# Optimization experiments

Measured on AMD Instinct MI355X. Metric: run time of the kernel, lower is better.

Reference implementation:

```python
import jax, jax.numpy as jnp
import numpy as np

N, C_IN, C_OUT, L, V, P, K, STRIDE = 8, 256, 256, 512, 25, 3, 9, 1
BN_EPS = 1e-5


def setup_inputs() -> dict:
    key = jax.random.key(0)
    k1, k2, k3, k4, k5 = jax.random.split(key, 5)
    x = jax.random.normal(k1, (N, C_IN, L, V), dtype=jnp.float32)
    # 1x1 Conv2d weight, no bias: (out_channels*num_partitions, in_channels)
    conv_w = jax.random.normal(k2, (C_OUT * P, C_IN), dtype=jnp.float32) * (1.0 / np.sqrt(C_IN))
    # adjacency (P, V, V)
    A = jax.random.normal(k3, (P, V, V), dtype=jnp.float32) * 0.2
    bn_gamma = jnp.ones((C_OUT,), dtype=jnp.float32)
    bn_beta = jnp.zeros((C_OUT,), dtype=jnp.float32)
    bn_mean = jax.random.normal(k4, (C_OUT,), dtype=jnp.float32) * 0.1
    bn_var = jax.random.uniform(k5, (C_OUT,), dtype=jnp.float32) + 0.5
    return {"x": x, "conv_w": conv_w, "A": A, "bn_gamma": bn_gamma,
            "bn_beta": bn_beta, "bn_mean": bn_mean, "bn_var": bn_var}


def reference(x, conv_w, A, bn_gamma, bn_beta, bn_mean, bn_var):
    # residual branch: identity (in_channels == out_channels, stride == 1)
    res = x
    # 1x1 conv: (N, C_in, L, V) -> (N, C_out*P, L, V)
    y = jnp.einsum('nclv,oc->nolv', x, conv_w)
    # split channels into P partitions, stack, permute -> (N, L, P, C_out, V)
    y = y.reshape(N, P, C_OUT, L, V).transpose(0, 3, 1, 2, 4)
    # graph aggregation: x @ A per partition
    y = jnp.einsum('nlpcv,pvw->nlpcw', y, A)
    # sum over partitions -> (N, L, C_out, V)
    s = y.sum(axis=2)
    # FIFO with zero init + strided taps == causal strided window sum:
    # out[t] = sum_{k=0}^{K-1} s[t - k*STRIDE], zero-padded for t-k*STRIDE < 0
    pad = (K - 1) * STRIDE
    s_pad = jnp.pad(s, ((0, 0), (pad, 0), (0, 0), (0, 0)))
    out = s_pad[:, 0:L]
    for k in range(1, K):
        out = out + s_pad[:, k * STRIDE:k * STRIDE + L]
    # stack along dim 2 in torch -> (N, C_out, L, V)
    out = out.transpose(0, 2, 1, 3)
    # BatchNorm2d (eval, running stats) + ReLU
    scale = bn_gamma * jax.lax.rsqrt(bn_var + BN_EPS)
    shift = bn_beta - bn_mean * scale
    out = out * scale[None, :, None, None] + shift[None, :, None, None]
    out = jax.nn.relu(out)
    # residual add, then ReLU (Dropout p=0.0 is identity)
    out = jax.nn.relu(out + res)
    return out
```

## Files before the change

### kernel.cpp

```cpp
#include <hip/hip_runtime.h>
#include <hip/hip_bf16.h>

#define NB 8
#define CC 256
#define OO 768
#define LL 512
#define VV 25
#define PP 3
#define KM 768
#define NKC 24
#define LT 4

typedef __attribute__((ext_vector_type(8))) short short8v;
typedef __attribute__((ext_vector_type(4))) float float4v;
typedef __attribute__((ext_vector_type(4))) int int4v;

__device__ inline unsigned pk2(float a, float b){
    __hip_bfloat16 ha = __float2bfloat16(a), hb = __float2bfloat16(b);
    unsigned short ua = *(unsigned short*)&ha, ub = *(unsigned short*)&hb;
    return (unsigned)ua | ((unsigned)ub << 16);
}

__global__ __launch_bounds__(256) void wperm_kernel(const float* __restrict__ W,
                                                    __hip_bfloat16* __restrict__ Wp) {
    int idx = blockIdx.x * 256 + threadIdx.x;
    if (idx >= OO * CC) return;
    int j    = idx & 7;
    int lane = (idx >> 3) & 63;
    int mt   = (idx >> 9) & 3;
    int wm   = (idx >> 11) & 3;
    int kc   = idx >> 13;
    int c = wm * 64 + mt * 16 + (lane & 15);
    int k = kc * 32 + ((lane >> 4) << 3) + j;
    int cib = k / 192;
    int r = k - cib * 192;
    int p = r >> 6;
    int ci = cib * 64 + (r & 63);
    Wp[idx] = __float2bfloat16(W[(p * 256 + c) * 256 + ci]);
}

__global__ __launch_bounds__(512, 4) void fused_main_kernel(
    const float* __restrict__ x,
    const __hip_bfloat16* __restrict__ Wp,
    const float* __restrict__ A,
    const float* __restrict__ gamma, const float* __restrict__ beta,
    const float* __restrict__ mean, const float* __restrict__ var,
    float* __restrict__ out)
{
    __shared__ __hip_bfloat16 Zb[2][128 * 32];
    __shared__ __hip_bfloat16 xsh[256 * 32];
    __shared__ __hip_bfloat16 a2t[3 * 32 * 32];
    __shared__ float scsh[512];

    const int tid  = threadIdx.x;
    const int lane = tid & 63, wid = tid >> 6;
    const int lcol = lane & 15, grp = lane >> 4;
    const int bid0 = blockIdx.x;
    const int swz = (bid0 & 7) * 128 + (bid0 >> 3);
    const int n  = swz >> 7;
    const int l0 = (swz & 127) * LT;
    const int wm = wid >> 1, wn = wid & 1;
    const int l_z = wid >> 1, mt_z = wid & 1;

    {
        int4v z = {0, 0, 0, 0};
        ((int4v*)xsh)[tid] = z;
        ((int4v*)xsh)[tid + 512] = z;
        if (tid < 384) ((int4v*)a2t)[tid] = z;
        int c = tid & 255;
        float sc = gamma[c] * rsqrtf(var[c] + 1e-5f);
        if (tid < 256) scsh[tid] = sc;
        else           scsh[tid] = beta[c] - mean[c] * sc;
    }
    __syncthreads();
    for (int idx = tid; idx < PP * VV * VV; idx += 512) {
        int p = idx / 625, r = idx - p * 625, v = r / 25, w = r - v * 25;
        int R = p * 32 + w;
        int e = (((v >> 3) ^ ((R >> 1) & 3)) << 3) | (v & 7);
        a2t[R * 32 + e] = __float2bfloat16(A[idx]);
    }

    auto stage_xs = [&](int cib) {
        for (int cc = tid; cc < 1600; cc += 512) {
            int ci6 = cc / 25, v = cc - ci6 * 25;
            const float* xp = x + ((size_t)(n * CC + cib * 64 + ci6) * LL) * VV + v;
            float rbuf[12];
            #pragma unroll
            for (int j = 0; j < 12; ++j) {
                int lj = l0 - 8 + j;
                rbuf[j] = (lj >= 0) ? xp[(size_t)lj * VV] : 0.f;
            }
            float wsv = 0.f;
            #pragma unroll
            for (int j = 0; j < 9; ++j) wsv += rbuf[j];
            #pragma unroll
            for (int i = 0; i < 4; ++i) {
                int R = ci6 * 4 + i;
                int e = (((v >> 3) ^ ((R >> 2) & 3)) << 3) | (v & 7);
                xsh[R * 32 + e] = __float2bfloat16(wsv);
                if (i < 3) wsv += rbuf[9 + i] - rbuf[i];
            }
        }
    };
    auto zgen = [&](int kc, int zbuf) {
        int p = (kc % 6) >> 1, h = kc & 1;
        int ci6 = h * 32 + mt_z * 16 + lcol;
        int R = ci6 * 4 + l_z;
        short8v az = *(const short8v*)&xsh[R * 32 + ((grp ^ ((R >> 2) & 3)) << 3)];
        #pragma unroll
        for (int wt = 0; wt < 2; ++wt) {
            int R2 = p * 32 + wt * 16 + lcol;
            short8v bz = *(const short8v*)&a2t[R2 * 32 + ((grp ^ ((R2 >> 1) & 3)) << 3)];
            float4v zc = {0.f, 0.f, 0.f, 0.f};
            zc = __builtin_amdgcn_mfma_f32_16x16x32_bf16(az, bz, zc, 0, 0, 0);
            int R3 = l_z * 32 + wt * 16 + lcol;
            int eb = (mt_z * 2 + (grp >> 1)) ^ ((R3 >> 1) & 3);
            unsigned* dst = (unsigned*)&Zb[zbuf][R3 * 32 + (eb << 3) + ((grp & 1) << 2)];
            dst[0] = pk2(zc[0], zc[1]);
            dst[1] = pk2(zc[2], zc[3]);
        }
    };

    float4v acc[4][4];
    #pragma unroll
    for (int i = 0; i < 4; ++i)
        #pragma unroll
        for (int j = 0; j < 4; ++j) acc[i][j] = (float4v){0.f, 0.f, 0.f, 0.f};

    const __hip_bfloat16* afbase = Wp + ((size_t)(wm * 4) * 64 + lane) * 8;

    #pragma unroll 1
    for (int cib = 0; cib < 4; ++cib) {
        stage_xs(cib);
        asm volatile("s_waitcnt lgkmcnt(0)" ::: "memory");
        __builtin_amdgcn_sched_barrier(0);
        __builtin_amdgcn_s_barrier();
        __builtin_amdgcn_sched_barrier(0);

        zgen(cib * 6, (cib * 6) & 1);
        asm volatile("s_waitcnt lgkmcnt(0)" ::: "memory");
        __builtin_amdgcn_sched_barrier(0);
        __builtin_amdgcn_s_barrier();
        __builtin_amdgcn_sched_barrier(0);

        #pragma unroll 1
        for (int j = 0; j < 6; ++j) {
            const int kc = cib * 6 + j;

            short8v af[4];
            {
                const __hip_bfloat16* ap = afbase + kc * 8192;
                #pragma unroll
                for (int mt = 0; mt < 4; ++mt)
                    af[mt] = *(const short8v*)(ap + mt * 512);
            }

            if (j < 5) zgen(kc + 1, (kc + 1) & 1);

            const __hip_bfloat16* zcur = &Zb[kc & 1][0];
            short8v bf[4];
            #pragma unroll
            for (int nt = 0; nt < 4; ++nt) {
                int R3 = wn * 64 + nt * 16 + lcol;
                bf[nt] = *(const short8v*)&zcur[R3 * 32 + ((grp ^ ((R3 >> 1) & 3)) << 3)];
            }

            __builtin_amdgcn_s_setprio(1);
            #pragma unroll
            for (int mt = 0; mt < 4; ++mt)
                #pragma unroll
                for (int nt = 0; nt < 4; ++nt)
                    acc[mt][nt] = __builtin_amdgcn_mfma_f32_16x16x32_bf16(af[mt], bf[nt], acc[mt][nt], 0, 0, 0);
            __builtin_amdgcn_s_setprio(0);

            asm volatile("s_waitcnt lgkmcnt(0)" ::: "memory");
            __builtin_amdgcn_sched_barrier(0);
            __builtin_amdgcn_s_barrier();
            __builtin_amdgcn_sched_barrier(0);
        }
    }

    #pragma unroll
    for (int mt = 0; mt < 4; ++mt) {
        #pragma unroll
        for (int nt = 0; nt < 4; ++nt) {
            int w = (wn * 64 + nt * 16) & 31;
            int l = l0 + ((wn * 64 + nt * 16) >> 5);
            int wl = w + lcol;
            if (wl < VV) {
                #pragma unroll
                for (int r = 0; r < 4; ++r) {
                    int c = wm * 64 + mt * 16 + grp * 4 + r;
                    float val = fmaf(acc[mt][nt][r], scsh[c], scsh[256 + c]);
                    val = fmaxf(val, 0.f);
                    size_t ad = ((size_t)(n * CC + c) * LL + l) * VV + wl;
                    val = fmaxf(val + x[ad], 0.f);
                    out[ad] = val;
                }
            }
        }
    }
}

__global__ __launch_bounds__(256) void wsum_kernel(const float* __restrict__ x,
                                                   float* __restrict__ xs) {
    const int CHUNKS = 8;
    int t = blockIdx.x * 256 + threadIdx.x;
    if (t >= NB * CC * VV * CHUNKS) return;
    int v = t % VV;
    int r = t / VV;
    int chunk = r % CHUNKS;
    int nc = r / CHUNKS;
    int l0 = chunk * (LL / CHUNKS);
    const float* xp = x  + (size_t)nc * (LL * VV) + v;
    float*       op = xs + (size_t)nc * (LL * VV) + v;
    float ring[8];
    float run = 0.f;
    #pragma unroll
    for (int k = 0; k < 8; ++k) {
        int j = l0 - 8 + k;
        float val = (j >= 0) ? xp[j * VV] : 0.f;
        ring[k] = val; run += val;
    }
    for (int base = l0; base < l0 + LL / CHUNKS; base += 8) {
        #pragma unroll
        for (int k = 0; k < 8; ++k) {
            int l = base + k;
            float val = xp[l * VV];
            float o = run + val;
            op[l * VV] = o;
            run = o - ring[k];
            ring[k] = val;
        }
    }
}

__global__ __launch_bounds__(256) void fused_fallback_kernel(
    const float* xs, const float* __restrict__ x, const float* __restrict__ W,
    const float* __restrict__ A,
    const float* __restrict__ gamma, const float* __restrict__ beta,
    const float* __restrict__ mean, const float* __restrict__ var,
    float* out)
{
    __shared__ float xshf[CC][28];
    const int bid = blockIdx.x;
    const int n = bid >> 9;
    const int l = bid & 511;
    const int tid = threadIdx.x;
    const size_t nbase = (size_t)n * CC * LL * VV;
    for (int k = tid; k < CC * VV; k += 256) {
        int ci = k / VV, v = k - ci * VV;
        xshf[ci][v] = xs[nbase + (size_t)ci * (LL * VV) + (size_t)l * VV + v];
    }
    __syncthreads();
    const int c = tid;
    float Y[PP * VV];
    #pragma unroll
    for (int i = 0; i < PP * VV; ++i) Y[i] = 0.f;
    const float* Wpr = W + c * 256;
    #pragma unroll 1
    for (int ci = 0; ci < CC; ++ci) {
        float xv[VV];
        #pragma unroll
        for (int v = 0; v < VV; ++v) xv[v] = xshf[ci][v];
        float w0 = Wpr[ci], w1 = Wpr[65536 + ci], w2 = Wpr[131072 + ci];
        #pragma unroll
        for (int v = 0; v < VV; ++v) Y[v]          = fmaf(w0, xv[v], Y[v]);
        #pragma unroll
        for (int v = 0; v < VV; ++v) Y[VV + v]     = fmaf(w1, xv[v], Y[VV + v]);
        #pragma unroll
        for (int v = 0; v < VV; ++v) Y[2 * VV + v] = fmaf(w2, xv[v], Y[2 * VV + v]);
    }
    float o[VV];
    #pragma unroll
    for (int w = 0; w < VV; ++w) o[w] = 0.f;
    #pragma unroll
    for (int p = 0; p < PP; ++p)
        #pragma unroll
        for (int v = 0; v < VV; ++v) {
            float y = Y[p * VV + v];
            const float* Ap = A + (p * VV + v) * VV;
            #pragma unroll
            for (int w = 0; w < VV; ++w) o[w] = fmaf(y, Ap[w], o[w]);
        }
    float sc = gamma[c] * rsqrtf(var[c] + 1e-5f);
    float sh = beta[c] - mean[c] * sc;
    const float* resp = x   + nbase + (size_t)c * (LL * VV) + (size_t)l * VV;
    float*       outp = out + nbase + (size_t)c * (LL * VV) + (size_t)l * VV;
    #pragma unroll
    for (int w = 0; w < VV; ++w) {
        float t2 = fmaf(o[w], sc, sh);
        t2 = fmaxf(t2, 0.f);
        t2 = fmaxf(t2 + resp[w], 0.f);
        outp[w] = t2;
    }
}

extern "C" void kernel_launch(void* const* d_in, const int* in_sizes, int n_in,
                              void* d_out, int out_size, void* d_ws, size_t ws_size,
                              hipStream_t stream) {
    const float* x  = (const float*)d_in[0];
    const float* W  = (const float*)d_in[1];
    const float* A  = (const float*)d_in[2];
    const float* gm = (const float*)d_in[3];
    const float* bt = (const float*)d_in[4];
    const float* mn = (const float*)d_in[5];
    const float* vr = (const float*)d_in[6];
    float* out = (float*)d_out;

    if (ws_size >= (size_t)(OO * CC * sizeof(__hip_bfloat16))) {
        __hip_bfloat16* Wp = (__hip_bfloat16*)d_ws;
        wperm_kernel<<<dim3((OO * CC + 255) / 256), dim3(256), 0, stream>>>(W, Wp);
        fused_main_kernel<<<dim3(NB * (LL / LT)), dim3(512), 0, stream>>>(
            x, Wp, A, gm, bt, mn, vr, out);
    } else {
        const int threadsA = NB * CC * VV * 8;
        wsum_kernel<<<dim3((threadsA + 255) / 256), dim3(256), 0, stream>>>(x, out);
        fused_fallback_kernel<<<dim3(NB * LL), dim3(256), 0, stream>>>(
            out, x, W, A, gm, bt, mn, vr, out);
    }
}
```

Before: 107.3 us.

## Halve L tile per block, use 4 waves, and double-buffer weight fragment loads

Each block now covers two time steps instead of four and runs 256 threads, with each of the four waves owning 64 output channels across the whole 64-column tile. This doubles the grid to 2048 blocks and roughly halves LDS use per block. Weight fragments for the next k-step are prefetched into a second register set while the current MFMAs run, and the setprio hints and trailing sched barriers are dropped. In exchange, each weight tile is reused across half as many columns, so weight traffic per output roughly doubles and more blocks re-read the x window halo.

```diff
diff --git a/kernel.cpp b/kernel.cpp
--- a/kernel.cpp
+++ b/kernel.cpp
@@ -9,7 +9,7 @@
 #define PP 3
 #define KM 768
 #define NKC 24
-#define LT 4
+#define LT 2
 
 typedef __attribute__((ext_vector_type(8))) short short8v;
 typedef __attribute__((ext_vector_type(4))) float float4v;
@@ -39,7 +39,7 @@
     Wp[idx] = __float2bfloat16(W[(p * 256 + c) * 256 + ci]);
 }
 
-__global__ __launch_bounds__(512, 4) void fused_main_kernel(
+__global__ __launch_bounds__(256, 4) void fused_main_kernel(
     const float* __restrict__ x,
     const __hip_bfloat16* __restrict__ Wp,
     const float* __restrict__ A,
@@ -47,8 +47,8 @@
     const float* __restrict__ mean, const float* __restrict__ var,
     float* __restrict__ out)
 {
-    __shared__ __hip_bfloat16 Zb[2][128 * 32];
-    __shared__ __hip_bfloat16 xsh[256 * 32];
+    __shared__ __hip_bfloat16 Zb[2][64 * 32];
+    __shared__ __hip_bfloat16 xsh[128 * 32];
     __shared__ __hip_bfloat16 a2t[3 * 32 * 32];
     __shared__ float scsh[512];
 
@@ -56,24 +56,24 @@
     const int lane = tid & 63, wid = tid >> 6;
     const int lcol = lane & 15, grp = lane >> 4;
     const int bid0 = blockIdx.x;
-    const int swz = (bid0 & 7) * 128 + (bid0 >> 3);
-    const int n  = swz >> 7;
-    const int l0 = (swz & 127) * LT;
-    const int wm = wid >> 1, wn = wid & 1;
-    const int l_z = wid >> 1, mt_z = wid & 1;
+    const int swz = (bid0 & 7) * 256 + (bid0 >> 3);
+    const int n  = swz >> 8;
+    const int l0 = (swz & 255) * LT;
+    const int wm = wid;
+    const int mt_z = wid & 1, l_z = wid >> 1;
 
     {
         int4v z = {0, 0, 0, 0};
         ((int4v*)xsh)[tid] = z;
-        ((int4v*)xsh)[tid + 512] = z;
-        if (tid < 384) ((int4v*)a2t)[tid] = z;
-        int c = tid & 255;
-        float sc = gamma[c] * rsqrtf(var[c] + 1e-5f);
-        if (tid < 256) scsh[tid] = sc;
-        else           scsh[tid] = beta[c] - mean[c] * sc;
+        ((int4v*)xsh)[tid + 256] = z;
+        ((int4v*)a2t)[tid] = z;
+        if (tid < 128) ((int4v*)a2t)[tid + 256] = z;
+        float sc = gamma[tid] * rsqrtf(var[tid] + 1e-5f);
+        scsh[tid] = sc;
+        scsh[256 + tid] = beta[tid] - mean[tid] * sc;
     }
     __syncthreads();
-    for (int idx = tid; idx < PP * VV * VV; idx += 512) {
+    for (int idx = tid; idx < PP * VV * VV; idx += 256) {
         int p = idx / 625, r = idx - p * 625, v = r / 25, w = r - v * 25;
         int R = p * 32 + w;
         int e = (((v >> 3) ^ ((R >> 1) & 3)) << 3) | (v & 7);
@@ -81,12 +81,12 @@
     }
 
     auto stage_xs = [&](int cib) {
-        for (int cc = tid; cc < 1600; cc += 512) {
+        for (int cc = tid; cc < 1600; cc += 256) {
             int ci6 = cc / 25, v = cc - ci6 * 25;
             const float* xp = x + ((size_t)(n * CC + cib * 64 + ci6) * LL) * VV + v;
-            float rbuf[12];
+            float rbuf[10];
             #pragma unroll
-            for (int j = 0; j < 12; ++j) {
+            for (int j = 0; j < 10; ++j) {
                 int lj = l0 - 8 + j;
                 rbuf[j] = (lj >= 0) ? xp[(size_t)lj * VV] : 0.f;
             }
@@ -94,19 +94,19 @@
             #pragma unroll
             for (int j = 0; j < 9; ++j) wsv += rbuf[j];
             #pragma unroll
-            for (int i = 0; i < 4; ++i) {
-                int R = ci6 * 4 + i;
-                int e = (((v >> 3) ^ ((R >> 2) & 3)) << 3) | (v & 7);
+            for (int i = 0; i < LT; ++i) {
+                int R = ci6 * LT + i;
+                int e = (((v >> 3) ^ ((R >> 1) & 3)) << 3) | (v & 7);
                 xsh[R * 32 + e] = __float2bfloat16(wsv);
-                if (i < 3) wsv += rbuf[9 + i] - rbuf[i];
+                if (i < LT - 1) wsv += rbuf[9 + i] - rbuf[i];
             }
         }
     };
     auto zgen = [&](int kc, int zbuf) {
         int p = (kc % 6) >> 1, h = kc & 1;
         int ci6 = h * 32 + mt_z * 16 + lcol;
-        int R = ci6 * 4 + l_z;
-        short8v az = *(const short8v*)&xsh[R * 32 + ((grp ^ ((R >> 2) & 3)) << 3)];
+        int R = ci6 * LT + l_z;
+        short8v az = *(const short8v*)&xsh[R * 32 + ((grp ^ ((R >> 1) & 3)) << 3)];
         #pragma unroll
         for (int wt = 0; wt < 2; ++wt) {
             int R2 = p * 32 + wt * 16 + lcol;
@@ -129,63 +129,64 @@
 
     const __hip_bfloat16* afbase = Wp + ((size_t)(wm * 4) * 64 + lane) * 8;
 
+#define KSTEP(kc, j, afc, afn) do {                                           \
+    if ((kc) + 1 < NKC) {                                                     \
+        const __hip_bfloat16* ap_ = afbase + (size_t)((kc) + 1) * 8192;       \
+        _Pragma("unroll")                                                     \
+        for (int mt_ = 0; mt_ < 4; ++mt_)                                     \
+            afn[mt_] = *(const short8v*)(ap_ + mt_ * 512);                    \
+    }                                                                         \
+    if ((j) < 5) zgen((kc) + 1, ((kc) + 1) & 1);                              \
+    {                                                                         \
+        const __hip_bfloat16* zcur_ = &Zb[(kc) & 1][0];                       \
+        short8v bf_[4];                                                       \
+        _Pragma("unroll")                                                     \
+        for (int nt_ = 0; nt_ < 4; ++nt_) {                                   \
+            int R3_ = nt_ * 16 + lcol;                                        \
+            bf_[nt_] = *(const short8v*)&zcur_[R3_ * 32 + ((grp ^ ((R3_ >> 1) & 3)) << 3)]; \
+        }                                                                     \
+        _Pragma("unroll")                                                     \
+        for (int mt_ = 0; mt_ < 4; ++mt_)                                     \
+            _Pragma("unroll")                                                 \
+            for (int nt_ = 0; nt_ < 4; ++nt_)                                 \
+                acc[mt_][nt_] = __builtin_amdgcn_mfma_f32_16x16x32_bf16(afc[mt_], bf_[nt_], acc[mt_][nt_], 0, 0, 0); \
+    }                                                                         \
+    asm volatile("s_waitcnt lgkmcnt(0)" ::: "memory");                        \
+    __builtin_amdgcn_sched_barrier(0);                                        \
+    __builtin_amdgcn_s_barrier();                                             \
+} while (0)
+
+    short8v afA[4], afB[4];
+    #pragma unroll
+    for (int mt = 0; mt < 4; ++mt) afA[mt] = *(const short8v*)(afbase + mt * 512);
+
     #pragma unroll 1
     for (int cib = 0; cib < 4; ++cib) {
         stage_xs(cib);
         asm volatile("s_waitcnt lgkmcnt(0)" ::: "memory");
         __builtin_amdgcn_sched_barrier(0);
         __builtin_amdgcn_s_barrier();
-        __builtin_amdgcn_sched_barrier(0);
 
         zgen(cib * 6, (cib * 6) & 1);
         asm volatile("s_waitcnt lgkmcnt(0)" ::: "memory");
         __builtin_amdgcn_sched_barrier(0);
         __builtin_amdgcn_s_barrier();
-        __builtin_amdgcn_sched_barrier(0);
 
         #pragma unroll 1
-        for (int j = 0; j < 6; ++j) {
-            const int kc = cib * 6 + j;
-
-            short8v af[4];
-            {
-                const __hip_bfloat16* ap = afbase + kc * 8192;
-                #pragma unroll
-                for (int mt = 0; mt < 4; ++mt)
-                    af[mt] = *(const short8v*)(ap + mt * 512);
-            }
-
-            if (j < 5) zgen(kc + 1, (kc + 1) & 1);
-
-            const __hip_bfloat16* zcur = &Zb[kc & 1][0];
-            short8v bf[4];
-            #pragma unroll
-            for (int nt = 0; nt < 4; ++nt) {
-                int R3 = wn * 64 + nt * 16 + lcol;
-                bf[nt] = *(const short8v*)&zcur[R3 * 32 + ((grp ^ ((R3 >> 1) & 3)) << 3)];
-            }
-
-            __builtin_amdgcn_s_setprio(1);
-            #pragma unroll
-            for (int mt = 0; mt < 4; ++mt)
-                #pragma unroll
-                for (int nt = 0; nt < 4; ++nt)
-                    acc[mt][nt] = __builtin_amdgcn_mfma_f32_16x16x32_bf16(af[mt], bf[nt], acc[mt][nt], 0, 0, 0);
-            __builtin_amdgcn_s_setprio(0);
-
-            asm volatile("s_waitcnt lgkmcnt(0)" ::: "memory");
-            __builtin_amdgcn_sched_barrier(0);
-            __builtin_amdgcn_s_barrier();
-            __builtin_amdgcn_sched_barrier(0);
-        }
-    }
+        for (int jj = 0; jj < 3; ++jj) {
+            KSTEP(cib * 6 + jj * 2,     jj * 2,     afA, afB);
+            KSTEP(cib * 6 + jj * 2 + 1, jj * 2 + 1, afB, afA);
+        }
+    }
+#undef KSTEP
 
     #pragma unroll
     for (int mt = 0; mt < 4; ++mt) {
         #pragma unroll
         for (int nt = 0; nt < 4; ++nt) {
-            int w = (wn * 64 + nt * 16) & 31;
-            int l = l0 + ((wn * 64 + nt * 16) >> 5);
+            int lw = nt * 16;
+            int w = lw & 31;
+            int l = l0 + (lw >> 5);
             int wl = w + lcol;
             if (wl < VV) {
                 #pragma unroll
@@ -311,7 +312,7 @@
     if (ws_size >= (size_t)(OO * CC * sizeof(__hip_bfloat16))) {
         __hip_bfloat16* Wp = (__hip_bfloat16*)d_ws;
         wperm_kernel<<<dim3((OO * CC + 255) / 256), dim3(256), 0, stream>>>(W, Wp);
-        fused_main_kernel<<<dim3(NB * (LL / LT)), dim3(512), 0, stream>>>(
+        fused_main_kernel<<<dim3(NB * (LL / LT)), dim3(256), 0, stream>>>(
             x, Wp, A, gm, bt, mn, vr, out);
     } else {
         const int threadsA = NB * CC * VV * 8;
```

New measurement: 115.1 us. 1.07x slower.

## Software-pipeline x staging and weight fragment loads across K-steps

Applied to the files above, without the earlier changes.

Prefetches the next channel block's x window sums from global memory into registers during the MFMA steps of the current block. The packed results are written to shared memory only after the block finishes, so global latency hides behind compute instead of sitting in a separate staging phase. Weight fragments are double-buffered so the next K-chunk loads while the current one feeds the MFMAs. Register pressure rises, so launch bounds drop from 4 to 3 waves per SIMD, which lowers occupancy.

```diff
diff --git a/kernel.cpp b/kernel.cpp
--- a/kernel.cpp
+++ b/kernel.cpp
@@ -39,7 +39,7 @@
     Wp[idx] = __float2bfloat16(W[(p * 256 + c) * 256 + ci]);
 }
 
-__global__ __launch_bounds__(512, 4) void fused_main_kernel(
+__global__ __launch_bounds__(512, 3) void fused_main_kernel(
     const float* __restrict__ x,
     const __hip_bfloat16* __restrict__ Wp,
     const float* __restrict__ A,
@@ -94,16 +94,15 @@
             #pragma unroll
             for (int j = 0; j < 9; ++j) wsv += rbuf[j];
             #pragma unroll
-            for (int i = 0; i < 4; ++i) {
+            for (int i = 0; i < LT; ++i) {
                 int R = ci6 * 4 + i;
                 int e = (((v >> 3) ^ ((R >> 2) & 3)) << 3) | (v & 7);
                 xsh[R * 32 + e] = __float2bfloat16(wsv);
-                if (i < 3) wsv += rbuf[9 + i] - rbuf[i];
+                if (i < LT - 1) wsv += rbuf[9 + i] - rbuf[i];
             }
         }
     };
-    auto zgen = [&](int kc, int zbuf) {
-        int p = (kc % 6) >> 1, h = kc & 1;
+    auto zgen = [&](int p, int h, int zbuf) {
         int ci6 = h * 32 + mt_z * 16 + lcol;
         int R = ci6 * 4 + l_z;
         short8v az = *(const short8v*)&xsh[R * 32 + ((grp ^ ((R >> 2) & 3)) << 3)];
@@ -128,64 +127,124 @@
         for (int j = 0; j < 4; ++j) acc[i][j] = (float4v){0.f, 0.f, 0.f, 0.f};
 
     const __hip_bfloat16* afbase = Wp + ((size_t)(wm * 4) * 64 + lane) * 8;
+    unsigned q[8];
+    short8v afA[4], afB[4];
+
+    stage_xs(0);
+    asm volatile("s_waitcnt lgkmcnt(0)" ::: "memory");
+    __builtin_amdgcn_sched_barrier(0);
+    __builtin_amdgcn_s_barrier();
+
+    zgen(0, 0, 0);
+    #pragma unroll
+    for (int mt = 0; mt < 4; ++mt) afA[mt] = *(const short8v*)(afbase + mt * 512);
+    asm volatile("s_waitcnt lgkmcnt(0)" ::: "memory");
+    __builtin_amdgcn_sched_barrier(0);
+    __builtin_amdgcn_s_barrier();
+
+#define KSTEP(J, IT, AFC, AFN) do {                                           \
+    const int kc_ = base + (J);                                               \
+    if (kc_ + 1 < NKC) {                                                      \
+        const __hip_bfloat16* ap_ = afbase + (size_t)(kc_ + 1) * 8192;        \
+        _Pragma("unroll")                                                     \
+        for (int mt_ = 0; mt_ < 4; ++mt_)                                     \
+            AFN[mt_] = *(const short8v*)(ap_ + mt_ * 512);                    \
+    }                                                                         \
+    float rb_[12]; int ci6_ = 0, v_ = 0; bool act_ = false;                   \
+    if ((IT) >= 0 && cib < 3) {                                               \
+        int cc_ = tid + (IT) * 512; act_ = cc_ < 1600;                        \
+        if (act_) {                                                           \
+            ci6_ = cc_ / 25; v_ = cc_ - ci6_ * 25;                            \
+            const float* xp_ = x + ((size_t)(n * CC + (cib + 1) * 64 + ci6_) * LL) * VV + v_; \
+            _Pragma("unroll")                                                 \
+            for (int jx_ = 0; jx_ < 12; ++jx_) {                              \
+                int lj_ = l0 - 8 + jx_;                                       \
+                rb_[jx_] = (lj_ >= 0) ? xp_[(size_t)lj_ * VV] : 0.f;          \
+            }                                                                 \
+        }                                                                     \
+    }                                                                         \
+    if ((J) < 5) zgen((((J) + 1) >> 1) & 3, ((J) + 1) & 1, ((J) + 1) & 1);    \
+    {                                                                         \
+        const __hip_bfloat16* zcur_ = &Zb[(J) & 1][0];                        \
+        short8v bf_[4];                                                       \
+        _Pragma("unroll")                                                     \
+        for (int nt_ = 0; nt_ < 4; ++nt_) {                                   \
+            int R3_ = wn * 64 + nt_ * 16 + lcol;                              \
+            bf_[nt_] = *(const short8v*)&zcur_[R3_ * 32 + ((grp ^ ((R3_ >> 1) & 3)) << 3)]; \
+        }                                                                     \
+        __builtin_amdgcn_s_setprio(1);                                        \
+        _Pragma("unroll")                                                     \
+        for (int mt_ = 0; mt_ < 4; ++mt_)                                     \
+            _Pragma("unroll")                                                 \
+            for (int nt_ = 0; nt_ < 4; ++nt_)                                 \
+                acc[mt_][nt_] = __builtin_amdgcn_mfma_f32_16x16x32_bf16(AFC[mt_], bf_[nt_], acc[mt_][nt_], 0, 0, 0); \
+        __builtin_amdgcn_s_setprio(0);                                        \
+    }                                                                         \
+    if ((IT) >= 0 && act_) {                                                  \
+        float w0_ = 0.f;                                                      \
+        _Pragma("unroll")                                                     \
+        for (int jx_ = 0; jx_ < 9; ++jx_) w0_ += rb_[jx_];                    \
+        float w1_ = w0_ + rb_[9]  - rb_[0];                                   \
+        float w2_ = w1_ + rb_[10] - rb_[1];                                   \
+        float w3_ = w2_ + rb_[11] - rb_[2];                                   \
+        q[(IT) * 2]     = pk2(w0_, w1_);                                      \
+        q[(IT) * 2 + 1] = pk2(w2_, w3_);                                      \
+    }                                                                         \
+    asm volatile("s_waitcnt lgkmcnt(0)" ::: "memory");                        \
+    __builtin_amdgcn_sched_barrier(0);                                        \
+    __builtin_amdgcn_s_barrier();                                             \
+} while (0)
 
     #pragma unroll 1
     for (int cib = 0; cib < 4; ++cib) {
-        stage_xs(cib);
-        asm volatile("s_waitcnt lgkmcnt(0)" ::: "memory");
-        __builtin_amdgcn_sched_barrier(0);
-        __builtin_amdgcn_s_barrier();
-        __builtin_amdgcn_sched_barrier(0);
-
-        zgen(cib * 6, (cib * 6) & 1);
-        asm volatile("s_waitcnt lgkmcnt(0)" ::: "memory");
-        __builtin_amdgcn_sched_barrier(0);
-        __builtin_amdgcn_s_barrier();
-        __builtin_amdgcn_sched_barrier(0);
-
-        #pragma unroll 1
-        for (int j = 0; j < 6; ++j) {
-            const int kc = cib * 6 + j;
-
-            short8v af[4];
-            {
-                const __hip_bfloat16* ap = afbase + kc * 8192;
-                #pragma unroll
-                for (int mt = 0; mt < 4; ++mt)
-                    af[mt] = *(const short8v*)(ap + mt * 512);
+        const int base = cib * 6;
+        KSTEP(0, -1, afA, afB);
+        KSTEP(1,  0, afB, afA);
+        KSTEP(2,  1, afA, afB);
+        KSTEP(3,  2, afB, afA);
+        KSTEP(4,  3, afA, afB);
+        KSTEP(5, -1, afB, afA);
+
+        if (cib < 3) {
+            #pragma unroll
+            for (int it = 0; it < 4; ++it) {
+                int cc = tid + it * 512;
+                if (cc < 1600) {
+                    int ci6 = cc / 25, v = cc - ci6 * 25;
+                    unsigned lo = q[it * 2], hi = q[it * 2 + 1];
+                    unsigned short hh0 = (unsigned short)(lo & 0xffff);
+                    unsigned short hh1 = (unsigned short)(lo >> 16);
+                    unsigned short hh2 = (unsigned short)(hi & 0xffff);
+                    unsigned short hh3 = (unsigned short)(hi >> 16);
+                    int e0 = (((v >> 3) ^ (((ci6 * 4 + 0) >> 2) & 3)) << 3) | (v & 7);
+                    *(unsigned short*)&xsh[(ci6 * 4 + 0) * 32 + e0] = hh0;
+                    int e1 = (((v >> 3) ^ (((ci6 * 4 + 1) >> 2) & 3)) << 3) | (v & 7);
+                    *(unsigned short*)&xsh[(ci6 * 4 + 1) * 32 + e1] = hh1;
+                    int e2 = (((v >> 3) ^ (((ci6 * 4 + 2) >> 2) & 3)) << 3) | (v & 7);
+                    *(unsigned short*)&xsh[(ci6 * 4 + 2) * 32 + e2] = hh2;
+                    int e3 = (((v >> 3) ^ (((ci6 * 4 + 3) >> 2) & 3)) << 3) | (v & 7);
+                    *(unsigned short*)&xsh[(ci6 * 4 + 3) * 32 + e3] = hh3;
+                }
             }
-
-            if (j < 5) zgen(kc + 1, (kc + 1) & 1);
-
-            const __hip_bfloat16* zcur = &Zb[kc & 1][0];
-            short8v bf[4];
-            #pragma unroll
-            for (int nt = 0; nt < 4; ++nt) {
-                int R3 = wn * 64 + nt * 16 + lcol;
-                bf[nt] = *(const short8v*)&zcur[R3 * 32 + ((grp ^ ((R3 >> 1) & 3)) << 3)];
-            }
-
-            __builtin_amdgcn_s_setprio(1);
-            #pragma unroll
-            for (int mt = 0; mt < 4; ++mt)
-                #pragma unroll
-                for (int nt = 0; nt < 4; ++nt)
-                    acc[mt][nt] = __builtin_amdgcn_mfma_f32_16x16x32_bf16(af[mt], bf[nt], acc[mt][nt], 0, 0, 0);
-            __builtin_amdgcn_s_setprio(0);
-
             asm volatile("s_waitcnt lgkmcnt(0)" ::: "memory");
             __builtin_amdgcn_sched_barrier(0);
             __builtin_amdgcn_s_barrier();
+
+            zgen(0, 0, 0);
+            asm volatile("s_waitcnt lgkmcnt(0)" ::: "memory");
             __builtin_amdgcn_sched_barrier(0);
-        }
-    }
+            __builtin_amdgcn_s_barrier();
+        }
+    }
+#undef KSTEP
 
     #pragma unroll
     for (int mt = 0; mt < 4; ++mt) {
         #pragma unroll
         for (int nt = 0; nt < 4; ++nt) {
-            int w = (wn * 64 + nt * 16) & 31;
-            int l = l0 + ((wn * 64 + nt * 16) >> 5);
+            int lw = (wn * 64 + nt * 16);
+            int w = lw & 31;
+            int l = l0 + (lw >> 5);
             int wl = w + lcol;
             if (wl < VV) {
                 #pragma unroll
```

Result: slower. 316.0 us (+194.4%).

## Precompute all six Z tiles per channel block to drop per-step barriers

Applied to the files above, without the earlier changes.

The graph-aggregation tiles for all three partitions and both channel halves are now produced at once into six LDS buffers per input-channel block. This replaces the double-buffered per-step generation, so the six inner GEMM steps run fully unrolled with no barrier between them. The intent is to cut barrier and sync overhead and give the compiler freedom to schedule the MFMA chain. In exchange the kernel uses more LDS, which can lower occupancy under the 512-thread, 4-block launch bound, and Z generation no longer overlaps with the GEMM. The setprio hints are also removed.

```diff
diff --git a/kernel.cpp b/kernel.cpp
--- a/kernel.cpp
+++ b/kernel.cpp
@@ -47,7 +47,7 @@
     const float* __restrict__ mean, const float* __restrict__ var,
     float* __restrict__ out)
 {
-    __shared__ __hip_bfloat16 Zb[2][128 * 32];
+    __shared__ __hip_bfloat16 Zb[6][128 * 32];
     __shared__ __hip_bfloat16 xsh[256 * 32];
     __shared__ __hip_bfloat16 a2t[3 * 32 * 32];
     __shared__ float scsh[512];
@@ -94,30 +94,40 @@
             #pragma unroll
             for (int j = 0; j < 9; ++j) wsv += rbuf[j];
             #pragma unroll
-            for (int i = 0; i < 4; ++i) {
+            for (int i = 0; i < LT; ++i) {
                 int R = ci6 * 4 + i;
                 int e = (((v >> 3) ^ ((R >> 2) & 3)) << 3) | (v & 7);
                 xsh[R * 32 + e] = __float2bfloat16(wsv);
-                if (i < 3) wsv += rbuf[9 + i] - rbuf[i];
+                if (i < LT - 1) wsv += rbuf[9 + i] - rbuf[i];
             }
         }
     };
-    auto zgen = [&](int kc, int zbuf) {
-        int p = (kc % 6) >> 1, h = kc & 1;
-        int ci6 = h * 32 + mt_z * 16 + lcol;
-        int R = ci6 * 4 + l_z;
-        short8v az = *(const short8v*)&xsh[R * 32 + ((grp ^ ((R >> 2) & 3)) << 3)];
-        #pragma unroll
-        for (int wt = 0; wt < 2; ++wt) {
-            int R2 = p * 32 + wt * 16 + lcol;
-            short8v bz = *(const short8v*)&a2t[R2 * 32 + ((grp ^ ((R2 >> 1) & 3)) << 3)];
-            float4v zc = {0.f, 0.f, 0.f, 0.f};
-            zc = __builtin_amdgcn_mfma_f32_16x16x32_bf16(az, bz, zc, 0, 0, 0);
-            int R3 = l_z * 32 + wt * 16 + lcol;
-            int eb = (mt_z * 2 + (grp >> 1)) ^ ((R3 >> 1) & 3);
-            unsigned* dst = (unsigned*)&Zb[zbuf][R3 * 32 + (eb << 3) + ((grp & 1) << 2)];
-            dst[0] = pk2(zc[0], zc[1]);
-            dst[1] = pk2(zc[2], zc[3]);
+
+    auto zgen_all = [&]() {
+        short8v az[2];
+        #pragma unroll
+        for (int h = 0; h < 2; ++h) {
+            int ci6 = h * 32 + mt_z * 16 + lcol;
+            int R = ci6 * 4 + l_z;
+            az[h] = *(const short8v*)&xsh[R * 32 + ((grp ^ ((R >> 2) & 3)) << 3)];
+        }
+        #pragma unroll
+        for (int p = 0; p < PP; ++p) {
+            #pragma unroll
+            for (int wt = 0; wt < 2; ++wt) {
+                int R2 = p * 32 + wt * 16 + lcol;
+                short8v bz = *(const short8v*)&a2t[R2 * 32 + ((grp ^ ((R2 >> 1) & 3)) << 3)];
+                #pragma unroll
+                for (int h = 0; h < 2; ++h) {
+                    float4v zc = {0.f, 0.f, 0.f, 0.f};
+                    zc = __builtin_amdgcn_mfma_f32_16x16x32_bf16(az[h], bz, zc, 0, 0, 0);
+                    int R3 = l_z * 32 + wt * 16 + lcol;
+                    int eb = (mt_z * 2 + (grp >> 1)) ^ ((R3 >> 1) & 3);
+                    unsigned* dst = (unsigned*)&Zb[p * 2 + h][R3 * 32 + (eb << 3) + ((grp & 1) << 2)];
+                    dst[0] = pk2(zc[0], zc[1]);
+                    dst[1] = pk2(zc[2], zc[3]);
+                }
+            }
         }
     };
 
@@ -131,52 +141,33 @@
 
     #pragma unroll 1
     for (int cib = 0; cib < 4; ++cib) {
+        __syncthreads();
         stage_xs(cib);
-        asm volatile("s_waitcnt lgkmcnt(0)" ::: "memory");
-        __builtin_amdgcn_sched_barrier(0);
-        __builtin_amdgcn_s_barrier();
-        __builtin_amdgcn_sched_barrier(0);
-
-        zgen(cib * 6, (cib * 6) & 1);
-        asm volatile("s_waitcnt lgkmcnt(0)" ::: "memory");
-        __builtin_amdgcn_sched_barrier(0);
-        __builtin_amdgcn_s_barrier();
-        __builtin_amdgcn_sched_barrier(0);
-
-        #pragma unroll 1
+        __syncthreads();
+        zgen_all();
+        __syncthreads();
+
+        #pragma unroll
         for (int j = 0; j < 6; ++j) {
             const int kc = cib * 6 + j;
-
             short8v af[4];
             {
-                const __hip_bfloat16* ap = afbase + kc * 8192;
+                const __hip_bfloat16* ap = afbase + (size_t)kc * 8192;
                 #pragma unroll
                 for (int mt = 0; mt < 4; ++mt)
                     af[mt] = *(const short8v*)(ap + mt * 512);
             }
-
-            if (j < 5) zgen(kc + 1, (kc + 1) & 1);
-
-            const __hip_bfloat16* zcur = &Zb[kc & 1][0];
             short8v bf[4];
             #pragma unroll
             for (int nt = 0; nt < 4; ++nt) {
                 int R3 = wn * 64 + nt * 16 + lcol;
-                bf[nt] = *(const short8v*)&zcur[R3 * 32 + ((grp ^ ((R3 >> 1) & 3)) << 3)];
-            }
-
-            __builtin_amdgcn_s_setprio(1);
+                bf[nt] = *(const short8v*)&Zb[j][R3 * 32 + ((grp ^ ((R3 >> 1) & 3)) << 3)];
+            }
             #pragma unroll
             for (int mt = 0; mt < 4; ++mt)
                 #pragma unroll
                 for (int nt = 0; nt < 4; ++nt)
                     acc[mt][nt] = __builtin_amdgcn_mfma_f32_16x16x32_bf16(af[mt], bf[nt], acc[mt][nt], 0, 0, 0);
-            __builtin_amdgcn_s_setprio(0);
-
-            asm volatile("s_waitcnt lgkmcnt(0)" ::: "memory");
-            __builtin_amdgcn_sched_barrier(0);
-            __builtin_amdgcn_s_barrier();
-            __builtin_amdgcn_sched_barrier(0);
         }
     }
 
@@ -184,8 +175,9 @@
     for (int mt = 0; mt < 4; ++mt) {
         #pragma unroll
         for (int nt = 0; nt < 4; ++nt) {
-            int w = (wn * 64 + nt * 16) & 31;
-            int l = l0 + ((wn * 64 + nt * 16) >> 5);
+            int lw = (wn * 64 + nt * 16);
+            int w = lw & 31;
+            int l = l0 + (lw >> 5);
             int wl = w + lcol;
             if (wl < VV) {
                 #pragma unroll
```

Measured after the change: 107.0 us. No clear change (-0.3%).
